# Kernel tuning notes

Measured on AMD Instinct MI355X. Metric: run time of the kernel, lower is better.

The kernel has to match this reference:

```python
import jax, jax.numpy as jnp
import numpy as np

E = 1024  # embed_dim
H = 16    # num_heads
D = E // H
L = 2048  # seq len (Q_len == K_len == V_len)


def setup_inputs() -> dict:
    key = jax.random.key(0)
    ks = jax.random.split(key, 12)
    w = lambda k, shape: jax.random.normal(k, shape, dtype=jnp.float32) * 0.02
    return {
        "V": jax.random.normal(ks[0], (L, E), dtype=jnp.float32),
        "K": jax.random.normal(ks[1], (L, E), dtype=jnp.float32),
        "Q": jax.random.normal(ks[2], (L, E), dtype=jnp.float32),
        "position": jnp.arange(L, dtype=jnp.float32).reshape(1, L),
        "W_q": w(ks[3], (E, E)),
        "W_k": w(ks[4], (E, E)),
        "W_v": w(ks[5], (E, E)),
        "W_k_rel": w(ks[6], (E, 1)),
        "W_v_rel": w(ks[7], (E, 1)),
        "W_k_abs": w(ks[8], (E, 1)),
        "W_v_abs": w(ks[9], (E, 1)),
        "W_out": w(ks[10], (E, E)),
        "b_out": jnp.zeros((E,), dtype=jnp.float32),
    }


def reference(V, K, Q, position, W_q, W_k, W_v, W_k_rel, W_v_rel,
              W_k_abs, W_v_abs, W_out, b_out):
    pos = position[0]                                   # [L]
    q = (Q @ W_q.T).reshape(L, H, D)                    # [L,H,D]
    k = (K @ W_k.T).reshape(L, H, D)
    v = (V @ W_v.T).reshape(L, H, D)

    # Absolute position bias. NOTE: the original computes log(pos+1)/10 but then
    # overwrites it with the raw position (a bug preserved here faithfully):
    # Linear(1,E) on a scalar == scalar * weight vector.
    v = v + (pos[:, None] * W_v_abs[:, 0][None, :]).reshape(L, H, D)
    k = k + (pos[:, None] * W_k_abs[:, 0][None, :]).reshape(L, H, D)

    energy = jnp.einsum('qhd,khd->hqk', q, k)           # [H,L,L]

    # Relative-position K bias: relative_position_K[q,j,h,d] = rel[q,j] * wK[h,d]
    # so einsum('nqhd,nhqjd->nhqj') reduces exactly to rel[q,j] * (Q[q,h]\cdot wK[h]).
    rel = jnp.clip(jnp.abs(pos[:, None] - pos[None, :]), 0.0, 5000.0) / 5000.0  # [L,L]
    wK = W_k_rel[:, 0].reshape(H, D)
    wV = W_v_rel[:, 0].reshape(H, D)
    qw = jnp.einsum('qhd,hd->hq', q, wK)                # [H,L]
    energy = energy + qw[:, :, None] * rel[None]

    # Original scales by sqrt(embed_dim), not sqrt(head_dim).
    attn = jax.nn.softmax(energy / jnp.sqrt(jnp.float32(E)), axis=-1)  # [H,L,L]

    out = jnp.einsum('hqk,khd->qhd', attn, v)           # [L,H,D]
    # Relative-position V: sum_j attn[h,q,j]*rel[q,j]*wV[h,d] == (attn*rel summed over j) outer wV.
    s = jnp.einsum('hqk,qk->hq', attn, rel)             # [H,L]
    out = out + jnp.einsum('hq,hd->qhd', s, wV)

    return out.reshape(L, E) @ W_out.T + b_out          # [L,E]
```

## Files before the change

kernel.cpp:

```cpp
#include <hip/hip_runtime.h>
#include <stdint.h>

#define LL 2048
#define EE 1024
#define HH 16
#define DD 64
#define KX 1056

using short8 = __attribute__((ext_vector_type(8))) short;
using s4v    = __attribute__((ext_vector_type(4))) short;
using f32x4  = __attribute__((ext_vector_type(4))) float;

#if __has_builtin(__builtin_amdgcn_mfma_f32_16x16x16_bf16)
#define MFMA16(a,b,c) __builtin_amdgcn_mfma_f32_16x16x16_bf16(a,b,c,0,0,0)
#elif __has_builtin(__builtin_amdgcn_mfma_f32_16x16x16bf16_1k)
#define MFMA16(a,b,c) __builtin_amdgcn_mfma_f32_16x16x16bf16_1k(a,b,c,0,0,0)
#else
static __device__ __forceinline__ f32x4 mfma16f(s4v a, s4v b, f32x4 c) {
  asm volatile("v_mfma_f32_16x16x16_bf16 %0, %1, %2, %0" : "+v"(c) : "v"(a), "v"(b));
  return c;
}
#define MFMA16(a,b,c) mfma16f(a,b,c)
#endif

__device__ __forceinline__ short f2bf(float x) {
  union { float f; uint32_t u; } v; v.f = x;
  uint32_t r = v.u + 0x7fffu + ((v.u >> 16) & 1u);
  return (short)(r >> 16);
}
__device__ __forceinline__ float bf2f(short s) {
  union { uint32_t u; float f; } v; v.u = ((uint32_t)(uint16_t)s) << 16;
  return v.f;
}

__device__ __forceinline__ void gld16(short* lds, const short* g) {
  __builtin_amdgcn_global_load_lds(
      (const __attribute__((address_space(1))) unsigned int*)g,
      (__attribute__((address_space(3))) unsigned int*)lds, 16, 0, 0);
}

#define NB_CONV 10240
__global__ __launch_bounds__(256) void convfused(
    const float* __restrict__ Q, const float* __restrict__ K,
    const float* __restrict__ V, const float* __restrict__ Wq,
    const float* __restrict__ Wk, const float* __restrict__ Wv,
    const float* __restrict__ Wout,
    const float* __restrict__ wka, const float* __restrict__ wkr,
    const float* __restrict__ wva, const float* __restrict__ wvr,
    short* __restrict__ Qb, short* __restrict__ Kb, short* __restrict__ Vb,
    short* __restrict__ Wqb, short* __restrict__ Wkb, short* __restrict__ Wvb,
    short* __restrict__ W2, float* __restrict__ u) {
  int b = blockIdx.x;
  if (b < NB_CONV) {
    const int S1 = LL * EE / 4;
    const int SW = EE * EE / 4;
    int i4 = b * 256 + threadIdx.x;
    const float* src; short* dst; int idx4; bool strided = false;
    if (i4 < 3 * S1) {
      int z = i4 >> 19; idx4 = i4 & (S1 - 1);
      src = z == 0 ? Q : (z == 1 ? K : V);
      dst = z == 0 ? Qb : (z == 1 ? Kb : Vb);
    } else {
      int j = i4 - 3 * S1;
      int z = j >> 18; idx4 = j & (SW - 1);
      src = z == 0 ? Wq : (z == 1 ? Wk : (z == 2 ? Wv : Wout));
      dst = z == 0 ? Wqb : (z == 1 ? Wkb : (z == 2 ? Wvb : W2));
      strided = (z == 3);
    }
    int i = idx4 * 4;
    const float4 v = *(const float4*)(src + i);
    int di = strided ? ((i >> 10) * KX + (i & 1023)) : i;
    union { short s[4]; uint64_t u; } p;
    p.s[0] = f2bf(v.x); p.s[1] = f2bf(v.y); p.s[2] = f2bf(v.z); p.s[3] = f2bf(v.w);
    *(uint64_t*)(dst + di) = p.u;
  } else if (b < NB_CONV + 128) {
    int flat = (b - NB_CONV) * 256 + threadIdx.x;
    int c = flat & (EE - 1);
    int h = (flat >> 10) & (HH - 1);
    int s = flat >> 14;
    const float* w = s ? wkr : wka;
    float acc = 0.f;
    #pragma unroll 8
    for (int d = 0; d < DD; ++d)
      acc += Wq[(size_t)(h * DD + d) * EE + c] * w[h * DD + d];
    u[flat] = acc;
  } else {
    int flat = (b - NB_CONV - 128) * 256 + threadIdx.x;
    int n = flat >> 5;
    int s = (flat >> 4) & 1;
    int h = flat & 15;
    const float* w = s ? wvr : wva;
    float acc = 0.f;
    #pragma unroll 8
    for (int d = 0; d < DD; ++d)
      acc += Wout[(size_t)n * EE + h * DD + d] * w[h * DD + d];
    W2[(size_t)n * KX + 1024 + s * 16 + h] = f2bf(acc);
  }
}

__global__ __launch_bounds__(256) void qawker(const float* __restrict__ Q,
                                              const float* __restrict__ u,
                                              float* __restrict__ qaw) {
  int i = blockIdx.x;
  int t = threadIdx.x;
  int h = t >> 4, seg = t & 15;
  const float* u0 = u + (size_t)h * EE;
  const float* u1 = u + (size_t)HH * EE + (size_t)h * EE;
  const float* q = Q + (size_t)i * EE;
  float a0 = 0.f, a1 = 0.f;
  for (int cc = 0; cc < 64; ++cc) {
    int c = cc * 16 + seg;
    float qv = q[c];
    a0 += qv * u0[c];
    a1 += qv * u1[c];
  }
  #pragma unroll
  for (int m = 1; m < 16; m <<= 1) {
    a0 += __shfl_xor(a0, m);
    a1 += __shfl_xor(a1, m);
  }
  if (seg == 0) { qaw[i * 32 + h] = a0; qaw[i * 32 + 16 + h] = a1; }
}

__global__ __launch_bounds__(256, 2) void gemm128(
    const short* __restrict__ Aall, const short* __restrict__ Ball,
    short* __restrict__ Call,
    int K, int aBatch, int bBatch, int cBatch,
    int ldc, int vTransZ, int ldcT, int scaleZ, float scaleVal)
{
  __shared__ __align__(16) short As[2][128 * 32];
  __shared__ __align__(16) short Bs[2][128 * 32];
  int z = blockIdx.z;
  const short* A = Aall + (size_t)z * aBatch;
  const short* B = Ball + (size_t)z * bBatch;
  int m0 = blockIdx.y * 128, n0 = blockIdx.x * 128;
  int t = threadIdx.x, lane = t & 63, w = t >> 6;
  int wm = w >> 1, wn = w & 1;
  int fr = lane & 15, g = lane >> 4, fo = g * 8;
  int lr = lane >> 2, lc = (lane & 3) * 8;
  const f32x4 vzero = {0.f, 0.f, 0.f, 0.f};
  f32x4 acc[4][4];
  #pragma unroll
  for (int i = 0; i < 4; ++i)
    #pragma unroll
    for (int j = 0; j < 4; ++j) acc[i][j] = vzero;

  int kTiles = K / 32;
  #pragma unroll
  for (int c = 0; c < 2; ++c) {
    int row = (w * 2 + c) * 16 + lr;
    gld16(&As[0][(w * 2 + c) * 512], A + (size_t)(m0 + row) * K + lc);
    gld16(&Bs[0][(w * 2 + c) * 512], B + (size_t)(n0 + row) * K + lc);
  }
  int cur = 0;
  for (int kt = 0; kt < kTiles; ++kt) {
    __syncthreads();
    if (kt + 1 < kTiles) {
      #pragma unroll
      for (int c = 0; c < 2; ++c) {
        int row = (w * 2 + c) * 16 + lr;
        gld16(&As[cur ^ 1][(w * 2 + c) * 512],
              A + (size_t)(m0 + row) * K + (kt + 1) * 32 + lc);
        gld16(&Bs[cur ^ 1][(w * 2 + c) * 512],
              B + (size_t)(n0 + row) * K + (kt + 1) * 32 + lc);
      }
    }
    short8 af[4], bf[4];
    #pragma unroll
    for (int i = 0; i < 4; ++i)
      af[i] = *(const short8*)&As[cur][(wm * 64 + i * 16 + fr) * 32 + fo];
    #pragma unroll
    for (int j = 0; j < 4; ++j)
      bf[j] = *(const short8*)&Bs[cur][(wn * 64 + j * 16 + fr) * 32 + fo];
    #pragma unroll
    for (int i = 0; i < 4; ++i)
      #pragma unroll
      for (int j = 0; j < 4; ++j)
        acc[i][j] = __builtin_amdgcn_mfma_f32_16x16x32_bf16(af[i], bf[j], acc[i][j], 0, 0, 0);
    cur ^= 1;
  }

  short* C = Call + (size_t)z * cBatch;
  bool doTrans = (z == vTransZ);
  bool doScale = (z == scaleZ);
  #pragma unroll
  for (int i = 0; i < 4; ++i) {
    #pragma unroll
    for (int j = 0; j < 4; ++j) {
      int n = n0 + wn * 64 + j * 16 + fr;
      #pragma unroll
      for (int r = 0; r < 4; ++r) {
        int m = m0 + wm * 64 + i * 16 + g * 4 + r;
        float val = acc[i][j][r];
        if (doScale) val *= scaleVal;
        if (doTrans) C[(size_t)n * ldcT + m] = f2bf(val);
        else         C[(size_t)m * ldc + n] = f2bf(val);
      }
    }
  }
}

__global__ __launch_bounds__(256, 2) void gemm_bt(
    const short* __restrict__ A, const short* __restrict__ B,
    float* __restrict__ C, int K, int ldc, const float* __restrict__ bias)
{
  __shared__ __align__(16) short As[2][64 * 32];
  __shared__ __align__(16) short Bs[2][128 * 32];
  int m0 = blockIdx.y * 64, n0 = blockIdx.x * 128;
  int t = threadIdx.x;
  int lane = t & 63, w = t >> 6;
  int wm = w >> 1, wn = w & 1;
  int fr = lane & 15, fo = (lane >> 4) * 8;
  int lr = lane >> 2, lc = (lane & 3) * 8;
  const f32x4 vzero = {0.f, 0.f, 0.f, 0.f};
  f32x4 acc[2][4];
  #pragma unroll
  for (int i = 0; i < 2; ++i)
    #pragma unroll
    for (int j = 0; j < 4; ++j) acc[i][j] = vzero;

  int kTiles = K / 32;
  {
    int arow = w * 16 + lr;
    gld16(&As[0][w * 512], A + (size_t)(m0 + arow) * K + lc);
    #pragma unroll
    for (int c = 0; c < 2; ++c) {
      int brow = (w * 2 + c) * 16 + lr;
      gld16(&Bs[0][(w * 2 + c) * 512], B + (size_t)(n0 + brow) * K + lc);
    }
  }
  int cur = 0;
  for (int kt = 0; kt < kTiles; ++kt) {
    __syncthreads();
    if (kt + 1 < kTiles) {
      int arow = w * 16 + lr;
      gld16(&As[cur ^ 1][w * 512], A + (size_t)(m0 + arow) * K + (kt + 1) * 32 + lc);
      #pragma unroll
      for (int c = 0; c < 2; ++c) {
        int brow = (w * 2 + c) * 16 + lr;
        gld16(&Bs[cur ^ 1][(w * 2 + c) * 512],
              B + (size_t)(n0 + brow) * K + (kt + 1) * 32 + lc);
      }
    }
    short8 af[2], bfr[4];
    #pragma unroll
    for (int i = 0; i < 2; ++i)
      af[i] = *(const short8*)&As[cur][(wm * 32 + i * 16 + fr) * 32 + fo];
    #pragma unroll
    for (int j = 0; j < 4; ++j)
      bfr[j] = *(const short8*)&Bs[cur][(wn * 64 + j * 16 + fr) * 32 + fo];
    #pragma unroll
    for (int i = 0; i < 2; ++i)
      #pragma unroll
      for (int j = 0; j < 4; ++j)
        acc[i][j] = __builtin_amdgcn_mfma_f32_16x16x32_bf16(af[i], bfr[j], acc[i][j], 0, 0, 0);
    cur ^= 1;
  }

  int rb = (lane >> 4) * 4;
  #pragma unroll
  for (int i = 0; i < 2; ++i) {
    #pragma unroll
    for (int j = 0; j < 4; ++j) {
      int n = n0 + wn * 64 + j * 16 + fr;
      float bv = bias[n];
      #pragma unroll
      for (int r = 0; r < 4; ++r) {
        int m = m0 + wm * 32 + i * 16 + rb + r;
        C[(size_t)m * ldc + n] = acc[i][j][r] + bv;
      }
    }
  }
}

__global__ __launch_bounds__(256, 4) void flash9(
    const short* __restrict__ qp, const short* __restrict__ kp,
    const short* __restrict__ vpT, const float* __restrict__ qaw,
    short* __restrict__ Obf, float* __restrict__ stats)
{
  __shared__ __align__(16) short lds[16384];
  int h = blockIdx.y;
  int q0 = blockIdx.x * 64;
  int split = blockIdx.z;
  int kbeg = split * 512;
  int t = threadIdx.x, w = t >> 6, lane = t & 63;
  int g = lane >> 4, fr = lane & 15;
  int gi = q0 + w * 16 + fr;
  float gif = (float)gi;
  float g4f = (float)(4 * g);
  const f32x4 vzero = {0.f, 0.f, 0.f, 0.f};

  int srow = lane >> 3;
  int schunk = (lane & 7) ^ srow;
  const short* ksrcA = kp + (size_t)(w * 16 + srow) * EE + h * 64 + schunk * 8;
  const short* ksrcB = ksrcA + (size_t)8 * EE;
  const short* vsrcA = vpT + (size_t)(h * 64 + w * 16 + srow) * LL + kbeg + schunk * 8;
  const short* vsrcB = vsrcA + (size_t)8 * LL;

  int fx = fr & 7;
  int kA0 = fr * 64 + ((g ^ fx) * 8);
  int kA1 = fr * 64 + (((g | 4) ^ fx) * 8);
  int g2 = g >> 1, gh = (g & 1) * 4;
  int vA[4];
  #pragma unroll
  for (int jt = 0; jt < 4; ++jt)
    vA[jt] = fr * 64 + (((2 * jt + g2) ^ fx) * 8) + gh;

  short8 qf[2];
  #pragma unroll
  for (int ks = 0; ks < 2; ++ks)
    qf[ks] = *(const short8*)(qp + (size_t)gi * EE + h * 64 + ks * 32 + g * 8);

  const float LOG2E = 1.4426950408889634f;
  const float sc = LOG2E / 32.f;
  float qa_s = qaw[gi * 32 + h] * sc;
  float qw_s = qaw[gi * 32 + 16 + h] * (sc / 5000.f);
  float qapw = qa_s + qw_s, qamw = qa_s - qw_s;

  float m2 = -1e30f, lsum = 0.f, SpA = 0.f, SrA = 0.f;
  f32x4 Oa[4];
  #pragma unroll
  for (int fc = 0; fc < 4; ++fc) Oa[fc] = vzero;

  {
    short* kb = lds;
    short* vb = lds + 4096;
    gld16(kb + w * 1024,       ksrcA + (size_t)kbeg * EE);
    gld16(kb + w * 1024 + 512, ksrcB + (size_t)kbeg * EE);
    gld16(vb + w * 1024,       vsrcA);
    gld16(vb + w * 1024 + 512, vsrcB);
  }

  int cur = 0;
  for (int kt = 0; kt < 8; ++kt) {
    int k0 = kbeg + kt * 64;
    float k0f = (float)k0;
    __syncthreads();

    if (kt < 7) {
      short* kb2 = lds + (cur ^ 1) * 8192;
      short* vb2 = kb2 + 4096;
      gld16(kb2 + w * 1024,       ksrcA + (size_t)(k0 + 64) * EE);
      gld16(kb2 + w * 1024 + 512, ksrcB + (size_t)(k0 + 64) * EE);
      gld16(vb2 + w * 1024,       vsrcA + (kt + 1) * 64);
      gld16(vb2 + w * 1024 + 512, vsrcB + (kt + 1) * 64);
    }
    const short* kb = lds + cur * 8192;
    const short* vb = kb + 4096;

    f32x4 St[4];
    #pragma unroll
    for (int jt = 0; jt < 4; ++jt) {
      f32x4 a = vzero;
      a = __builtin_amdgcn_mfma_f32_16x16x32_bf16(
              *(const short8*)(kb + jt * 1024 + kA0), qf[0], a, 0, 0, 0);
      a = __builtin_amdgcn_mfma_f32_16x16x32_bf16(
              *(const short8*)(kb + jt * 1024 + kA1), qf[1], a, 0, 0, 0);
      St[jt] = a;
    }

    float pf[4][4];
    float tmv = -1e30f;
    if (k0 < q0) {
      float b4 = fmaf(g4f, qamw, k0f * qa_s + (gif - k0f) * qw_s);
      #pragma unroll
      for (int jt = 0; jt < 4; ++jt)
        #pragma unroll
        for (int r = 0; r < 4; ++r) {
          float e = St[jt][r] + fmaf((float)(jt * 16 + r), qamw, b4);
          pf[jt][r] = e;
          tmv = fmaxf(tmv, e);
        }
    } else if (k0 > q0) {
      float b4 = fmaf(g4f, qapw, k0f * qa_s + (k0f - gif) * qw_s);
      #pragma unroll
      for (int jt = 0; jt < 4; ++jt)
        #pragma unroll
        for (int r = 0; r < 4; ++r) {
          float e = St[jt][r] + fmaf((float)(jt * 16 + r), qapw, b4);
          pf[jt][r] = e;
          tmv = fmaxf(tmv, e);
        }
    } else {
      #pragma unroll
      for (int jt = 0; jt < 4; ++jt)
        #pragma unroll
        for (int r = 0; r < 4; ++r) {
          float jgf = k0f + g4f + (float)(jt * 16 + r);
          float e = St[jt][r] + jgf * qa_s + fabsf(gif - jgf) * qw_s;
          pf[jt][r] = e;
          tmv = fmaxf(tmv, e);
        }
    }
    tmv = fmaxf(tmv, __shfl_xor(tmv, 16));
    tmv = fmaxf(tmv, __shfl_xor(tmv, 32));

    if (__any(tmv > m2 + 8.f)) {
      float mn = fmaxf(m2, tmv);
      float alpha = exp2f(m2 - mn);
      m2 = mn;
      lsum *= alpha; SpA *= alpha; SrA *= alpha;
      #pragma unroll
      for (int r = 0; r < 4; ++r) {
        float alr = __shfl(alpha, ((lane >> 4) << 2) + r);
        #pragma unroll
        for (int fc = 0; fc < 4; ++fc) Oa[fc][r] *= alr;
      }
    }

    float Pt = 0.f, S1 = 0.f;
    #pragma unroll
    for (int jt = 0; jt < 4; ++jt)
      #pragma unroll
      for (int r = 0; r < 4; ++r) {
        float p = exp2f(pf[jt][r] - m2);
        pf[jt][r] = p;
        Pt += p;
        S1 = fmaf(p, (float)(jt * 16 + r), S1);
      }
    float jbase = k0f + g4f;
    lsum += Pt;
    SpA += fmaf(jbase, Pt, S1);
    if (k0 > q0)       SrA += fmaf(jbase - gif, Pt, S1);
    else if (k0 < q0)  SrA -= fmaf(jbase - gif, Pt, S1);
    else {
      #pragma unroll
      for (int jt = 0; jt < 4; ++jt)
        #pragma unroll
        for (int r = 0; r < 4; ++r)
          SrA = fmaf(pf[jt][r], fabsf(gif - (jbase + (float)(jt * 16 + r))), SrA);
    }

    s4v pa[4];
    #pragma unroll
    for (int jt = 0; jt < 4; ++jt) {
      int lo, hi;
      asm("v_cvt_pk_bf16_f32 %0, %1, %2" : "=v"(lo) : "v"(pf[jt][0]), "v"(pf[jt][1]));
      asm("v_cvt_pk_bf16_f32 %0, %1, %2" : "=v"(hi) : "v"(pf[jt][2]), "v"(pf[jt][3]));
      union { int i[2]; s4v s; } uu; uu.i[0] = lo; uu.i[1] = hi;
      pa[jt] = uu.s;
    }

    #pragma unroll
    for (int jt = 0; jt < 4; ++jt) {
      #pragma unroll
      for (int fc = 0; fc < 4; ++fc) {
        s4v vv = *(const s4v*)(vb + fc * 1024 + vA[jt]);
        Oa[fc] = MFMA16(pa[jt], vv, Oa[fc]);
      }
    }
    cur ^= 1;
  }

  lsum += __shfl_xor(lsum, 16); lsum += __shfl_xor(lsum, 32);
  SpA  += __shfl_xor(SpA, 16);  SpA  += __shfl_xor(SpA, 32);
  SrA  += __shfl_xor(SrA, 16);  SrA  += __shfl_xor(SrA, 32);

  size_t sb = (size_t)(split * HH + h) * LL;
  if (g == 0) {
    float4 s4 = {m2, lsum, SpA, SrA};
    *(float4*)&stats[(sb + q0 + w * 16 + fr) * 4] = s4;
  }

  float linv = 1.f / lsum;
  #pragma unroll
  for (int r = 0; r < 4; ++r) {
    int q = q0 + w * 16 + 4 * g + r;
    float il = __shfl(linv, 4 * g + r);
    union { short s[4]; uint64_t u; } pk;
    #pragma unroll
    for (int fc = 0; fc < 4; ++fc) pk.s[fc] = f2bf(Oa[fc][r] * il);
    *(uint64_t*)&Obf[(sb + q) * 64 + fr * 4] = pk.u;
  }
}

__global__ __launch_bounds__(256) void merge4(const short* __restrict__ Obf,
                                              const float* __restrict__ stats,
                                              short* __restrict__ X2) {
  int q = blockIdx.x;
  int t = threadIdx.x;
  int h = t >> 4, ds = (t & 15) * 4;
  float4 s[4];
  #pragma unroll
  for (int i = 0; i < 4; ++i)
    s[i] = *(const float4*)&stats[((size_t)(i * HH + h) * LL + q) * 4];
  float m = fmaxf(fmaxf(s[0].x, s[1].x), fmaxf(s[2].x, s[3].x));
  float a[4], denom = 0.f;
  #pragma unroll
  for (int i = 0; i < 4; ++i) { a[i] = exp2f(s[i].x - m); denom += a[i] * s[i].y; }
  float invd = 1.f / denom;
  float acc[4] = {0.f, 0.f, 0.f, 0.f};
  #pragma unroll
  for (int i = 0; i < 4; ++i) {
    float wgt = a[i] * s[i].y * invd;
    const short* ob = &Obf[((size_t)(i * HH + h) * LL + q) * 64];
    #pragma unroll
    for (int e = 0; e < 4; ++e) {
      int d = ds + e;
      int pidx = (d & 15) * 4 + (d >> 4);
      acc[e] = fmaf(wgt, bf2f(ob[pidx]), acc[e]);
    }
  }
  union { short s[4]; uint64_t u; } pk;
  #pragma unroll
  for (int e = 0; e < 4; ++e) pk.s[e] = f2bf(acc[e]);
  *(uint64_t*)&X2[(size_t)q * KX + h * 64 + ds] = pk.u;

  if (t < 32) {
    int hh = t & 15;
    float4 ts[4];
    float mm = -1e30f;
    #pragma unroll
    for (int i = 0; i < 4; ++i) {
      ts[i] = *(const float4*)&stats[((size_t)(i * HH + hh) * LL + q) * 4];
      mm = fmaxf(mm, ts[i].x);
    }
    float num = 0.f, den = 0.f;
    #pragma unroll
    for (int i = 0; i < 4; ++i) {
      float ai = exp2f(ts[i].x - mm);
      den += ai * ts[i].y;
      num += ai * ((t < 16) ? ts[i].z : ts[i].w);
    }
    float val = num / den;
    if (t >= 16) val *= (1.f / 5000.f);
    X2[(size_t)q * KX + 1024 + (t < 16 ? hh : 16 + hh)] = f2bf(val);
  }
}

extern "C" void kernel_launch(void* const* d_in, const int* in_sizes, int n_in,
                              void* d_out, int out_size, void* d_ws, size_t ws_size,
                              hipStream_t stream) {
  const float* V    = (const float*)d_in[0];
  const float* Kin  = (const float*)d_in[1];
  const float* Q    = (const float*)d_in[2];
  const float* Wq   = (const float*)d_in[4];
  const float* Wk   = (const float*)d_in[5];
  const float* Wv   = (const float*)d_in[6];
  const float* Wkr  = (const float*)d_in[7];
  const float* Wvr  = (const float*)d_in[8];
  const float* Wka  = (const float*)d_in[9];
  const float* Wva  = (const float*)d_in[10];
  const float* Wout = (const float*)d_in[11];
  const float* bout = (const float*)d_in[12];

  char* ws = (char*)d_ws;
  size_t off = 0;
  auto alloc = [&](size_t bytes) -> void* {
    void* p = ws + off;
    off = (off + bytes + 255) & ~(size_t)255;
    return p;
  };
  short* Qb  = (short*)alloc((size_t)LL * EE * 2);
  short* Kb  = (short*)alloc((size_t)LL * EE * 2);
  short* Vb  = (short*)alloc((size_t)LL * EE * 2);
  short* Wqb = (short*)alloc((size_t)EE * EE * 2);
  short* Wkb = (short*)alloc((size_t)EE * EE * 2);
  short* Wvb = (short*)alloc((size_t)EE * EE * 2);
  short* qp  = (short*)alloc((size_t)LL * EE * 2);
  short* kp  = (short*)alloc((size_t)LL * EE * 2);
  short* vpT = (short*)alloc((size_t)EE * LL * 2);
  short* W2  = (short*)alloc((size_t)EE * KX * 2);
  short* X2  = (short*)alloc((size_t)LL * KX * 2);
  float* u   = (float*)alloc((size_t)2 * HH * EE * 4);
  float* qaw = (float*)alloc((size_t)LL * 32 * 4);
  short* Obf   = Qb;
  float* stats = (float*)((char*)Qb + (size_t)16777216);
  (void)in_sizes; (void)n_in; (void)out_size; (void)ws_size;

  const float sc = 1.4426950408889634f / 32.f;

  convfused<<<NB_CONV + 256, 256, 0, stream>>>(
      Q, Kin, V, Wq, Wk, Wv, Wout, Wka, Wkr, Wva, Wvr,
      Qb, Kb, Vb, Wqb, Wkb, Wvb, W2, u);

  qawker<<<LL, 256, 0, stream>>>(Q, u, qaw);

  dim3 gp(EE / 128, LL / 128, 3);
  gemm128<<<gp, 256, 0, stream>>>(Qb, Wqb, qp, EE,
                                  LL * EE, EE * EE, LL * EE,
                                  EE, 2, LL,
                                  0, sc);

  flash9<<<dim3(LL / 64, HH, 4), 256, 0, stream>>>(qp, kp, vpT, qaw, Obf, stats);

  merge4<<<LL, 256, 0, stream>>>(Obf, stats, X2);

  dim3 go(EE / 128, LL / 64);
  gemm_bt<<<go, 256, 0, stream>>>(X2, W2, (float*)d_out, KX, EE, bout);
}
```

Before: 147.6 us.

## Fuse qaw into projection GEMM, stage V transpose via LDS, halve flash splits

Merges the qaw dot-product kernel into the projection GEMM launch as extra blocks, removing one launch and letting the two overlap. The transposed V store is now staged through swizzled shared memory so global writes are coalesced 16-byte stores instead of scattered 2-byte writes. The flash attention key split drops from 4 to 2, so each block covers 1024 keys. That halves the partial outputs and merge work, but the grid is halved and occupancy may drop.

```diff
diff --git a/kernel.cpp b/kernel.cpp
--- a/kernel.cpp
+++ b/kernel.cpp
@@ -98,43 +98,48 @@
   }
 }
 
-__global__ __launch_bounds__(256) void qawker(const float* __restrict__ Q,
-                                              const float* __restrict__ u,
-                                              float* __restrict__ qaw) {
-  int i = blockIdx.x;
-  int t = threadIdx.x;
-  int h = t >> 4, seg = t & 15;
-  const float* u0 = u + (size_t)h * EE;
-  const float* u1 = u + (size_t)HH * EE + (size_t)h * EE;
-  const float* q = Q + (size_t)i * EE;
-  float a0 = 0.f, a1 = 0.f;
-  for (int cc = 0; cc < 64; ++cc) {
-    int c = cc * 16 + seg;
-    float qv = q[c];
-    a0 += qv * u0[c];
-    a1 += qv * u1[c];
-  }
-  #pragma unroll
-  for (int m = 1; m < 16; m <<= 1) {
-    a0 += __shfl_xor(a0, m);
-    a1 += __shfl_xor(a1, m);
-  }
-  if (seg == 0) { qaw[i * 32 + h] = a0; qaw[i * 32 + 16 + h] = a1; }
-}
-
-__global__ __launch_bounds__(256, 2) void gemm128(
+__global__ __launch_bounds__(256, 2) void projqaw(
     const short* __restrict__ Aall, const short* __restrict__ Ball,
     short* __restrict__ Call,
     int K, int aBatch, int bBatch, int cBatch,
-    int ldc, int vTransZ, int ldcT, int scaleZ, float scaleVal)
+    int ldc, int vTransZ, int ldcT, int scaleZ, float scaleVal,
+    const float* __restrict__ Qf, const float* __restrict__ u,
+    float* __restrict__ qaw)
 {
-  __shared__ __align__(16) short As[2][128 * 32];
-  __shared__ __align__(16) short Bs[2][128 * 32];
-  int z = blockIdx.z;
+  __shared__ __align__(16) short smem[16384];
+  int b = blockIdx.x;
+  int t = threadIdx.x;
+
+  if (b >= 384) {
+    int i = b - 384;
+    int h = t >> 4, seg = t & 15;
+    const float* u0 = u + (size_t)h * EE;
+    const float* u1 = u + (size_t)HH * EE + (size_t)h * EE;
+    const float* q = Qf + (size_t)i * EE;
+    float a0 = 0.f, a1 = 0.f;
+    for (int cc = 0; cc < 64; ++cc) {
+      int c = cc * 16 + seg;
+      float qv = q[c];
+      a0 += qv * u0[c];
+      a1 += qv * u1[c];
+    }
+    #pragma unroll
+    for (int m = 1; m < 16; m <<= 1) {
+      a0 += __shfl_xor(a0, m);
+      a1 += __shfl_xor(a1, m);
+    }
+    if (seg == 0) { qaw[i * 32 + h] = a0; qaw[i * 32 + 16 + h] = a1; }
+    return;
+  }
+
+  short* As0 = smem;
+  short* Bs0 = smem + 8192;
+  int z = b / 128;
+  int rem = b % 128;
+  int n0 = (rem & 7) * 128, m0 = (rem >> 3) * 128;
   const short* A = Aall + (size_t)z * aBatch;
   const short* B = Ball + (size_t)z * bBatch;
-  int m0 = blockIdx.y * 128, n0 = blockIdx.x * 128;
-  int t = threadIdx.x, lane = t & 63, w = t >> 6;
+  int lane = t & 63, w = t >> 6;
   int wm = w >> 1, wn = w & 1;
   int fr = lane & 15, g = lane >> 4, fo = g * 8;
   int lr = lane >> 2, lc = (lane & 3) * 8;
@@ -149,8 +154,8 @@
   #pragma unroll
   for (int c = 0; c < 2; ++c) {
     int row = (w * 2 + c) * 16 + lr;
-    gld16(&As[0][(w * 2 + c) * 512], A + (size_t)(m0 + row) * K + lc);
-    gld16(&Bs[0][(w * 2 + c) * 512], B + (size_t)(n0 + row) * K + lc);
+    gld16(&As0[(w * 2 + c) * 512], A + (size_t)(m0 + row) * K + lc);
+    gld16(&Bs0[(w * 2 + c) * 512], B + (size_t)(n0 + row) * K + lc);
   }
   int cur = 0;
   for (int kt = 0; kt < kTiles; ++kt) {
@@ -159,19 +164,19 @@
       #pragma unroll
       for (int c = 0; c < 2; ++c) {
         int row = (w * 2 + c) * 16 + lr;
-        gld16(&As[cur ^ 1][(w * 2 + c) * 512],
+        gld16(&As0[(cur ^ 1) * 4096 + (w * 2 + c) * 512],
               A + (size_t)(m0 + row) * K + (kt + 1) * 32 + lc);
-        gld16(&Bs[cur ^ 1][(w * 2 + c) * 512],
+        gld16(&Bs0[(cur ^ 1) * 4096 + (w * 2 + c) * 512],
               B + (size_t)(n0 + row) * K + (kt + 1) * 32 + lc);
       }
     }
     short8 af[4], bf[4];
     #pragma unroll
     for (int i = 0; i < 4; ++i)
-      af[i] = *(const short8*)&As[cur][(wm * 64 + i * 16 + fr) * 32 + fo];
+      af[i] = *(const short8*)&As0[cur * 4096 + (wm * 64 + i * 16 + fr) * 32 + fo];
     #pragma unroll
     for (int j = 0; j < 4; ++j)
-      bf[j] = *(const short8*)&Bs[cur][(wn * 64 + j * 16 + fr) * 32 + fo];
+      bf[j] = *(const short8*)&Bs0[cur * 4096 + (wn * 64 + j * 16 + fr) * 32 + fo];
     #pragma unroll
     for (int i = 0; i < 4; ++i)
       #pragma unroll
@@ -181,8 +186,45 @@
   }
 
   short* C = Call + (size_t)z * cBatch;
-  bool doTrans = (z == vTransZ);
   bool doScale = (z == scaleZ);
+
+  if (z == vTransZ) {
+    __syncthreads();
+    for (int half = 0; half < 2; ++half) {
+      if (wn == half) {
+        #pragma unroll
+        for (int i = 0; i < 4; ++i) {
+          #pragma unroll
+          for (int j = 0; j < 4; ++j) {
+            int nl = j * 16 + fr;
+            int chunk = wm * 16 + i * 4 + g;
+            union { short s[4]; uint64_t u; } pk;
+            #pragma unroll
+            for (int r = 0; r < 4; ++r) {
+              float val = acc[i][j][r];
+              if (doScale) val *= scaleVal;
+              pk.s[r] = f2bf(val);
+            }
+            *(uint64_t*)&smem[nl * 128 + (chunk ^ (nl & 15)) * 4] = pk.u;
+          }
+        }
+      }
+      __syncthreads();
+      int row = t >> 2, seg = t & 3;
+      int nglob = n0 + half * 64 + row;
+      #pragma unroll
+      for (int cc = 0; cc < 4; ++cc) {
+        int mc2 = seg * 4 + cc;
+        uint64_t lo = *(uint64_t*)&smem[row * 128 + ((mc2 * 2)     ^ (row & 15)) * 4];
+        uint64_t hi = *(uint64_t*)&smem[row * 128 + ((mc2 * 2 + 1) ^ (row & 15)) * 4];
+        union { uint64_t q[2]; int4 v; } st; st.q[0] = lo; st.q[1] = hi;
+        *(int4*)(C + (size_t)nglob * ldcT + m0 + mc2 * 8) = st.v;
+      }
+      __syncthreads();
+    }
+    return;
+  }
+
   #pragma unroll
   for (int i = 0; i < 4; ++i) {
     #pragma unroll
@@ -193,8 +235,7 @@
         int m = m0 + wm * 64 + i * 16 + g * 4 + r;
         float val = acc[i][j][r];
         if (doScale) val *= scaleVal;
-        if (doTrans) C[(size_t)n * ldcT + m] = f2bf(val);
-        else         C[(size_t)m * ldc + n] = f2bf(val);
+        C[(size_t)m * ldc + n] = f2bf(val);
       }
     }
   }
@@ -273,7 +314,7 @@
   }
 }
 
-__global__ __launch_bounds__(256, 4) void flash9(
+__global__ __launch_bounds__(256, 4) void flash10(
     const short* __restrict__ qp, const short* __restrict__ kp,
     const short* __restrict__ vpT, const float* __restrict__ qaw,
     short* __restrict__ Obf, float* __restrict__ stats)
@@ -282,7 +323,7 @@
   int h = blockIdx.y;
   int q0 = blockIdx.x * 64;
   int split = blockIdx.z;
-  int kbeg = split * 512;
+  int kbeg = split * 1024;
   int t = threadIdx.x, w = t >> 6, lane = t & 63;
   int g = lane >> 4, fr = lane & 15;
   int gi = q0 + w * 16 + fr;
@@ -332,12 +373,12 @@
   }
 
   int cur = 0;
-  for (int kt = 0; kt < 8; ++kt) {
+  for (int kt = 0; kt < 16; ++kt) {
     int k0 = kbeg + kt * 64;
     float k0f = (float)k0;
     __syncthreads();
 
-    if (kt < 7) {
+    if (kt < 15) {
       short* kb2 = lds + (cur ^ 1) * 8192;
       short* vb2 = kb2 + 4096;
       gld16(kb2 + w * 1024,       ksrcA + (size_t)(k0 + 64) * EE);
@@ -474,24 +515,24 @@
   }
 }
 
-__global__ __launch_bounds__(256) void merge4(const short* __restrict__ Obf,
+__global__ __launch_bounds__(256) void merge2(const short* __restrict__ Obf,
                                               const float* __restrict__ stats,
                                               short* __restrict__ X2) {
   int q = blockIdx.x;
   int t = threadIdx.x;
   int h = t >> 4, ds = (t & 15) * 4;
-  float4 s[4];
-  #pragma unroll
-  for (int i = 0; i < 4; ++i)
+  float4 s[2];
+  #pragma unroll
+  for (int i = 0; i < 2; ++i)
     s[i] = *(const float4*)&stats[((size_t)(i * HH + h) * LL + q) * 4];
-  float m = fmaxf(fmaxf(s[0].x, s[1].x), fmaxf(s[2].x, s[3].x));
-  float a[4], denom = 0.f;
-  #pragma unroll
-  for (int i = 0; i < 4; ++i) { a[i] = exp2f(s[i].x - m); denom += a[i] * s[i].y; }
+  float m = fmaxf(s[0].x, s[1].x);
+  float a[2], denom = 0.f;
+  #pragma unroll
+  for (int i = 0; i < 2; ++i) { a[i] = exp2f(s[i].x - m); denom += a[i] * s[i].y; }
   float invd = 1.f / denom;
   float acc[4] = {0.f, 0.f, 0.f, 0.f};
   #pragma unroll
-  for (int i = 0; i < 4; ++i) {
+  for (int i = 0; i < 2; ++i) {
     float wgt = a[i] * s[i].y * invd;
     const short* ob = &Obf[((size_t)(i * HH + h) * LL + q) * 64];
     #pragma unroll
@@ -508,16 +549,16 @@
 
   if (t < 32) {
     int hh = t & 15;
-    float4 ts[4];
+    float4 ts[2];
     float mm = -1e30f;
     #pragma unroll
-    for (int i = 0; i < 4; ++i) {
+    for (int i = 0; i < 2; ++i) {
       ts[i] = *(const float4*)&stats[((size_t)(i * HH + hh) * LL + q) * 4];
       mm = fmaxf(mm, ts[i].x);
     }
     float num = 0.f, den = 0.f;
     #pragma unroll
-    for (int i = 0; i < 4; ++i) {
+    for (int i = 0; i < 2; ++i) {
       float ai = exp2f(ts[i].x - mm);
       den += ai * ts[i].y;
       num += ai * ((t < 16) ? ts[i].z : ts[i].w);
@@ -574,17 +615,15 @@
       Q, Kin, V, Wq, Wk, Wv, Wout, Wka, Wkr, Wva, Wvr,
       Qb, Kb, Vb, Wqb, Wkb, Wvb, W2, u);
 
-  qawker<<<LL, 256, 0, stream>>>(Q, u, qaw);
-
-  dim3 gp(EE / 128, LL / 128, 3);
-  gemm128<<<gp, 256, 0, stream>>>(Qb, Wqb, qp, EE,
-                                  LL * EE, EE * EE, LL * EE,
-                                  EE, 2, LL,
-                                  0, sc);
-
-  flash9<<<dim3(LL / 64, HH, 4), 256, 0, stream>>>(qp, kp, vpT, qaw, Obf, stats);
-
-  merge4<<<LL, 256, 0, stream>>>(Obf, stats, X2);
+  projqaw<<<384 + LL, 256, 0, stream>>>(Qb, Wqb, qp, EE,
+                                        LL * EE, EE * EE, LL * EE,
+                                        EE, 2, LL,
+                                        0, sc,
+                                        Q, u, qaw);
+
+  flash10<<<dim3(LL / 64, HH, 2), 256, 0, stream>>>(qp, kp, vpT, qaw, Obf, stats);
+
+  merge2<<<LL, 256, 0, stream>>>(Obf, stats, X2);
 
   dim3 go(EE / 128, LL / 64);
   gemm_bt<<<go, 256, 0, stream>>>(X2, W2, (float*)d_out, KX, EE, bout);
```

Result: faster. 129.3 us (-12.4%).
